# Optimization experiments

Hardware: AMD Instinct MI355X
Metric: run time of the kernel (lower is better)

The kernel has to match this reference:

```python
import jax, jax.numpy as jnp
import numpy as np
from jax.scipy.special import logsumexp

B, N, C = 64, 1024, 558
NUM_ITERS = 20
TEMP = 1.0
CLASS_W = 1.0
ASSIGN_W = 0.5
NEG_INF = -1e30  # grad-safe stand-in for float('-inf') used by the torch code
EPS = 1e-8


def setup_inputs() -> dict:
    key = jax.random.key(0)
    k1, k2, k3, k4 = jax.random.split(key, 4)
    logits = jax.random.normal(k1, (B, N, C), dtype=jnp.float32)
    labels = jax.random.randint(k2, (B, N), 0, C, dtype=jnp.int32)
    visible_mask = jax.random.uniform(k3, (B, N)) < 0.9
    visible_mask = visible_mask.at[:, 0].set(True)  # every worm has >=1 visible node
    dustbin_score = jnp.asarray(-1.0, dtype=jnp.float32)  # nn.Parameter(-1.0)
    return {"logits": logits, "dustbin_score": dustbin_score,
            "labels": labels, "visible_mask": visible_mask}


def _log_sinkhorn(log_scores, log_mu, log_nu, iters):
    # log_scores: [B, N, M]; log_mu: [B, N]; log_nu: [B, M]
    log_u0 = jnp.zeros(log_scores.shape[:2], jnp.float32)
    log_v0 = jnp.zeros((log_scores.shape[0], log_scores.shape[2]), jnp.float32)

    def step(carry, _):
        log_u, log_v = carry
        log_u = log_mu - logsumexp(log_scores + log_v[:, None, :], axis=-1)
        log_v = log_nu - logsumexp(log_scores + log_u[:, :, None], axis=1)
        return (log_u, log_v), None

    (log_u, log_v), _ = jax.lax.scan(step, (log_u0, log_v0), None, length=iters)
    return jnp.exp(log_scores + log_u[:, :, None] + log_v[:, None, :])


def reference(logits, dustbin_score, labels, visible_mask):
    log_probs = jax.nn.log_softmax(logits, axis=-1)  # [B, N, C]

    # ---- Matcher (one_to_one=False) ----
    log_scores = log_probs / TEMP
    dust = jnp.broadcast_to(dustbin_score / TEMP, (B, N, 1))
    ls = jnp.concatenate([log_scores, dust], axis=-1)  # [B, N, C+1]

    maskf = visible_mask.astype(jnp.float32)
    nvis = maskf.sum(axis=1)  # [B], >= 1 by construction
    log_mu = jnp.where(visible_mask, -jnp.log(nvis)[:, None], NEG_INF)  # [B, N]
    log_nu = jnp.full((B, C + 1), -jnp.log(jnp.float32(C + 1)))  # uniform marginals

    P = _log_sinkhorn(ls, log_mu, log_nu, NUM_ITERS)  # [B, N, C+1]
    soft = P[:, :, :-1]  # drop dustbin column -> [B, N, C]

    # ---- classification loss (worm-averaged NLL, label_smoothing=0) ----
    # labels are packed at the front: visible node with rank r uses labels[b, r]
    ranks = jnp.clip(jnp.cumsum(visible_mask.astype(jnp.int32), axis=1) - 1, 0)
    tgt = jnp.take_along_axis(labels, ranks, axis=1)  # [B, N]
    nll = -jnp.take_along_axis(log_probs, tgt[..., None], axis=2)[..., 0]  # [B, N]
    class_loss = ((nll * maskf).sum(axis=1) / nvis).mean()

    # ---- assignment confidence loss (worm-averaged entropy) ----
    ent = -(soft * jnp.log(soft + EPS)).sum(axis=-1)  # [B, N]
    assignment_loss = ((ent * maskf).sum(axis=1) / nvis).mean()

    total_loss = CLASS_W * class_loss + ASSIGN_W * assignment_loss
    return total_loss


if __name__ == "__main__":
    print(reference(**setup_inputs()))
```

## Files before the change

### kernel.cpp

```cpp
#include <hip/hip_runtime.h>

#define Bb 64
#define Nn 1024
#define Cc 558
#define CP1 559
#define CPAD 560
#define ITERS 20
#define PBLK 8
#define RPB (Nn/PBLK)
#define WAVES 8
#define RPW (RPB/WAVES)
#define BLOCK 512

#if __has_builtin(__builtin_amdgcn_rcpf)
#define RCP(x) __builtin_amdgcn_rcpf(x)
#else
#define RCP(x) (1.0f / (x))
#endif

__device__ __forceinline__ float wave_sum(float v) {
#pragma unroll
    for (int off = 32; off > 0; off >>= 1) v += __shfl_xor(v, off, 64);
    return v;
}
__device__ __forceinline__ float wave_max(float v) {
#pragma unroll
    for (int off = 32; off > 0; off >>= 1) v = fmaxf(v, __shfl_xor(v, off, 64));
    return v;
}

#if __has_builtin(__builtin_amdgcn_cvt_pk_fp8_f32) && __has_builtin(__builtin_amdgcn_cvt_pk_f32_fp8)
#define HW_FP8 1
typedef float v2f __attribute__((ext_vector_type(2)));
#endif

__device__ __forceinline__ unsigned enc1_sw(float v) {
    if (!(v > 0.f)) return 0u;
    unsigned u = __float_as_uint(v);
    unsigned t = u + 0x7FFFFu + ((u >> 20) & 1u);
    int e = (int)(t >> 23) - 120;
    if (e < 1) return 0u;
    if (e > 15) return 0x7Eu;
    return ((unsigned)e << 3) | ((t >> 20) & 7u);
}
__device__ __forceinline__ float dec1_sw(unsigned b8) {
    return b8 ? __uint_as_float((((b8 >> 3) + 120u) << 23) | ((b8 & 7u) << 20)) : 0.f;
}
__device__ __forceinline__ unsigned enc4(float f0, float f1, float f2, float f3) {
#ifdef HW_FP8
    int w = 0;
    w = __builtin_amdgcn_cvt_pk_fp8_f32(f0, f1, w, false);
    w = __builtin_amdgcn_cvt_pk_fp8_f32(f2, f3, w, true);
    return (unsigned)w;
#else
    return enc1_sw(f0) | (enc1_sw(f1) << 8) | (enc1_sw(f2) << 16) | (enc1_sw(f3) << 24);
#endif
}
__device__ __forceinline__ void dec4(unsigned w, float& f0, float& f1, float& f2, float& f3) {
#ifdef HW_FP8
    v2f a = __builtin_amdgcn_cvt_pk_f32_fp8((int)w, false);
    v2f b = __builtin_amdgcn_cvt_pk_f32_fp8((int)w, true);
    f0 = a[0]; f1 = a[1]; f2 = b[0]; f3 = b[1];
#else
    f0 = dec1_sw(w & 0xffu); f1 = dec1_sw((w >> 8) & 0xffu);
    f2 = dec1_sw((w >> 16) & 0xffu); f3 = dec1_sw(w >> 24);
#endif
}
__device__ __forceinline__ float dec1(unsigned b8) {
#ifdef HW_FP8
    v2f a = __builtin_amdgcn_cvt_pk_f32_fp8((int)b8, false);
    return a[0];
#else
    return dec1_sw(b8);
#endif
}

__global__ __launch_bounds__(256) void k0_softmax(const float* __restrict__ logits,
        const float* __restrict__ dustbin, unsigned char* __restrict__ p8,
        float* __restrict__ qd, float* __restrict__ lse) {
    const int wave = threadIdx.x >> 6, lane = threadIdx.x & 63;
    const int r = (blockIdx.x << 2) + wave;
    const float* rowp = logits + (size_t)r * Cc;
    const bool tl = lane < 46;
    const float e0 = __expf(rowp[lane]);
    const float e1 = __expf(rowp[64 + lane]);
    const float e2 = __expf(rowp[128 + lane]);
    const float e3 = __expf(rowp[192 + lane]);
    const float e4 = __expf(rowp[256 + lane]);
    const float e5 = __expf(rowp[320 + lane]);
    const float e6 = __expf(rowp[384 + lane]);
    const float e7 = __expf(rowp[448 + lane]);
    float et = 0.f;
    if (tl) et = __expf(rowp[512 + lane]);
    float mx = fmaxf(fmaxf(fmaxf(e0, e1), fmaxf(e2, e3)),
                     fmaxf(fmaxf(e4, e5), fmaxf(e6, e7)));
    mx = wave_max(fmaxf(mx, et));
    const float s = wave_sum(e0 + e1 + e2 + e3 + e4 + e5 + e6 + e7 + et);
    const float fm = 416.f * RCP(mx);
    const unsigned w0 = enc4(e0 * fm, e1 * fm, e2 * fm, e3 * fm);
    const unsigned w1 = enc4(e4 * fm, e5 * fm, e6 * fm, e7 * fm);
    unsigned char* rowq = p8 + (size_t)r * CPAD;
    *(unsigned long long*)(rowq + (lane << 3)) =
        (unsigned long long)w0 | ((unsigned long long)w1 << 32);
    if (tl) rowq[512 + lane] = (unsigned char)(enc4(et * fm, 0.f, 0.f, 0.f) & 0xffu);
    if (lane == 0) {
        qd[r] = __expf(dustbin[0]) * fm * s;
        lse[r] = __logf(s);
    }
}

__global__ __launch_bounds__(256) void k1_batch(const float* __restrict__ logits,
        const int* __restrict__ labels, const void* __restrict__ maskp,
        const float* __restrict__ lse, float* __restrict__ class_part,
        float* __restrict__ inv_nvis, unsigned char* __restrict__ visc) {
    const int b = blockIdx.x, tid = threadIdx.x;
    __shared__ int sF, sB;
    __shared__ int cs_[256];
    __shared__ float red[256];
    if (tid == 0) { sF = 0; sB = 0; }
    __syncthreads();
    {
        const unsigned int* mw = (const unsigned int*)maskp;
        int lF = 0, lB = 0;
        for (int i = tid; i < (Bb * Nn) / 4; i += 256) {
            unsigned w = mw[i];
            if (w == 0x3F800000u) lF = 1;
            else if (w > 1u) lB = 1;
        }
        if (lF) sF = 1;
        if (lB) sB = 1;
    }
    __syncthreads();
    const int mode = sF ? 2 : (sB ? 1 : 0);
    int v[4]; int local = 0;
#pragma unroll
    for (int j = 0; j < 4; ++j) {
        const int n = tid * 4 + j;
        const int idx = b * Nn + n;
        int m;
        if (mode == 1)      m = ((const unsigned char*)maskp)[idx] != 0;
        else if (mode == 2) m = ((const float*)maskp)[idx] != 0.f;
        else                m = ((const int*)maskp)[idx] != 0;
        v[j] = m; local += m;
    }
    cs_[tid] = local;
    __syncthreads();
    for (int off = 1; off < 256; off <<= 1) {
        int x = 0;
        if (tid >= off) x = cs_[tid - off];
        __syncthreads();
        cs_[tid] += x;
        __syncthreads();
    }
    const int nvis = cs_[255];
    int run = cs_[tid] - local;
    float nllsum = 0.f;
#pragma unroll
    for (int j = 0; j < 4; ++j) {
        const int n = tid * 4 + j;
        run += v[j];
        visc[b * Nn + n] = (unsigned char)v[j];
        if (v[j]) {
            const int tgt = labels[b * Nn + (run - 1)];
            nllsum += lse[b * Nn + n] - logits[((size_t)(b * Nn + n)) * Cc + tgt];
        }
    }
    red[tid] = nllsum;
    __syncthreads();
    for (int off = 128; off > 0; off >>= 1) {
        if (tid < off) red[tid] += red[tid + off];
        __syncthreads();
    }
    if (tid == 0) {
        class_part[b] = red[0] / (float)nvis;
        inv_nvis[b] = 1.f / (float)nvis;
    }
}

__global__ __launch_bounds__(BLOCK) void k2_iter(const unsigned char* __restrict__ p8,
        const float* __restrict__ qd, const unsigned char* __restrict__ visc,
        const float* __restrict__ inv_nvis, float* __restrict__ eu_g,
        const float* __restrict__ Rp, float* __restrict__ Wp, const int first) {
    __shared__ float evl[CPAD];
    __shared__ float partl[WAVES][CPAD];
    const int b = blockIdx.x >> 3, p = blockIdx.x & 7, tid = threadIdx.x;
    const int wave = tid >> 6, lane = tid & 63;
    for (int c = tid; c < CP1; c += BLOCK) {
        float ev = 1.f;
        if (!first) {
            const float* CSr = Rp + (size_t)(b * PBLK) * CPAD + c;
            float s = 0.f;
#pragma unroll
            for (int q = 0; q < PBLK; ++q) s += CSr[q * CPAD];
            ev = RCP(559.f * s);
        }
        evl[c] = ev;
    }
    __syncthreads();
    const bool tl = lane < 46;
    const float evr0 = evl[lane],        evr1 = evl[64 + lane];
    const float evr2 = evl[128 + lane],  evr3 = evl[192 + lane];
    const float evr4 = evl[256 + lane],  evr5 = evl[320 + lane];
    const float evr6 = evl[384 + lane],  evr7 = evl[448 + lane];
    const float evt = tl ? evl[512 + lane] : 0.f;
    const float evd = evl[558];
    const float invn = inv_nvis[b];
    const int row0 = (b << 10) + (p << 7) + (wave << 4);
    const uint4 vA = *(const uint4*)(visc + row0);
    const unsigned vw[4] = {vA.x, vA.y, vA.z, vA.w};
#define VISB(r) ((vw[(r) >> 2] >> (((r) & 3) << 3)) & 0xffu)
    float pc0 = 0.f, pc1 = 0.f, pc2 = 0.f, pc3 = 0.f;
    float pc4 = 0.f, pc5 = 0.f, pc6 = 0.f, pc7 = 0.f;
    float pct = 0.f, pcd = 0.f;
#pragma unroll
    for (int r = 0; r < RPW; ++r) {
        const unsigned char* rowq = p8 + (size_t)(row0 + r) * CPAD;
        const unsigned long long wq = *(const unsigned long long*)(rowq + (lane << 3));
        float f0, f1, f2, f3, f4, f5, f6, f7;
        dec4((unsigned)wq, f0, f1, f2, f3);
        dec4((unsigned)(wq >> 32), f4, f5, f6, f7);
        float xt = 0.f;
        if (tl) xt = dec1(rowq[512 + lane]);
        const float qdr = qd[row0 + r];
        float s = f0 * evr0 + f1 * evr1 + f2 * evr2 + f3 * evr3
                + f4 * evr4 + f5 * evr5 + f6 * evr6 + f7 * evr7 + xt * evt;
        s = wave_sum(s) + qdr * evd;
        const float euv = VISB(r) ? invn * RCP(s) : 0.f;
        if (lane == 0) eu_g[row0 + r] = euv;
        pc0 += f0 * euv; pc1 += f1 * euv; pc2 += f2 * euv; pc3 += f3 * euv;
        pc4 += f4 * euv; pc5 += f5 * euv; pc6 += f6 * euv; pc7 += f7 * euv;
        pct += xt * euv; pcd += qdr * euv;
    }
    partl[wave][lane] = pc0;        partl[wave][64 + lane] = pc1;
    partl[wave][128 + lane] = pc2;  partl[wave][192 + lane] = pc3;
    partl[wave][256 + lane] = pc4;  partl[wave][320 + lane] = pc5;
    partl[wave][384 + lane] = pc6;  partl[wave][448 + lane] = pc7;
    if (tl) partl[wave][512 + lane] = pct;
    if (lane == 0) partl[wave][558] = pcd;
    __syncthreads();
    float* CSw = Wp + (size_t)(b * PBLK + p) * CPAD;
    for (int c = tid; c < CP1; c += BLOCK) {
        CSw[c] = partl[0][c] + partl[1][c] + partl[2][c] + partl[3][c]
               + partl[4][c] + partl[5][c] + partl[6][c] + partl[7][c];
    }
}

__global__ __launch_bounds__(BLOCK) void k3_final(const unsigned char* __restrict__ p8,
        const float* __restrict__ eu_g, const float* __restrict__ Rp,
        const float* __restrict__ inv_nvis, float* __restrict__ assign_part) {
    __shared__ float evl[CPAD];
    __shared__ float red[WAVES];
    const int b = blockIdx.x >> 3, p = blockIdx.x & 7, tid = threadIdx.x;
    const int wave = tid >> 6, lane = tid & 63;
    for (int c = tid; c < CP1; c += BLOCK) {
        const float* CSr = Rp + (size_t)(b * PBLK) * CPAD + c;
        float s = 0.f;
#pragma unroll
        for (int q = 0; q < PBLK; ++q) s += CSr[q * CPAD];
        evl[c] = RCP(559.f * s);
    }
    __syncthreads();
    const bool tl = lane < 46;
    const float evr0 = evl[lane],        evr1 = evl[64 + lane];
    const float evr2 = evl[128 + lane],  evr3 = evl[192 + lane];
    const float evr4 = evl[256 + lane],  evr5 = evl[320 + lane];
    const float evr6 = evl[384 + lane],  evr7 = evl[448 + lane];
    const float evt = tl ? evl[512 + lane] : 0.f;
    const int row0 = (b << 10) + (p << 7) + (wave << 4);
    float acc = 0.f;
#pragma unroll
    for (int r = 0; r < RPW; ++r) {
        const float euv = eu_g[row0 + r];
        const unsigned char* rowq = p8 + (size_t)(row0 + r) * CPAD;
        const unsigned long long wq = *(const unsigned long long*)(rowq + (lane << 3));
        float f0, f1, f2, f3, f4, f5, f6, f7;
        dec4((unsigned)wq, f0, f1, f2, f3);
        dec4((unsigned)(wq >> 32), f4, f5, f6, f7);
        float xt = 0.f;
        if (tl) xt = dec1(rowq[512 + lane]);
        float P;
        P = f0 * euv * evr0; acc -= P * __logf(P + 1e-8f);
        P = f1 * euv * evr1; acc -= P * __logf(P + 1e-8f);
        P = f2 * euv * evr2; acc -= P * __logf(P + 1e-8f);
        P = f3 * euv * evr3; acc -= P * __logf(P + 1e-8f);
        P = f4 * euv * evr4; acc -= P * __logf(P + 1e-8f);
        P = f5 * euv * evr5; acc -= P * __logf(P + 1e-8f);
        P = f6 * euv * evr6; acc -= P * __logf(P + 1e-8f);
        P = f7 * euv * evr7; acc -= P * __logf(P + 1e-8f);
        P = xt * euv * evt;  acc -= P * __logf(P + 1e-8f);
    }
    acc = wave_sum(acc);
    if (lane == 0) red[wave] = acc;
    __syncthreads();
    if (tid == 0) {
        float s = 0.f;
#pragma unroll
        for (int w = 0; w < WAVES; ++w) s += red[w];
        assign_part[blockIdx.x] = s * inv_nvis[b];
    }
}

__global__ void k4_out(const float* __restrict__ class_part,
                       const float* __restrict__ assign_part, float* __restrict__ out) {
    const int b = threadIdx.x;
    float v = class_part[b];
    float a = 0.f;
#pragma unroll
    for (int p = 0; p < PBLK; ++p) a += assign_part[b * PBLK + p];
    v += 0.5f * a;
    v = wave_sum(v);
    if (b == 0) out[0] = v * (1.f / 64.f);
}

extern "C" void kernel_launch(void* const* d_in, const int* in_sizes, int n_in,
                              void* d_out, int out_size, void* d_ws, size_t ws_size,
                              hipStream_t stream) {
    const float* logits = (const float*)d_in[0];
    const float* dustbin = (const float*)d_in[1];
    const int* labels = (const int*)d_in[2];
    const void* mask = d_in[3];
    float* out = (float*)d_out;

    char* ws = (char*)d_ws;
    size_t off = 0;
    unsigned char* p8 = (unsigned char*)(ws + off); off += (size_t)Bb * Nn * CPAD;
    float* qd = (float*)(ws + off);            off += (size_t)Bb * Nn * 4;
    float* lse = (float*)(ws + off);           off += (size_t)Bb * Nn * 4;
    float* eu_g = (float*)(ws + off);          off += (size_t)Bb * Nn * 4;
    unsigned char* visc = (unsigned char*)(ws + off); off += (size_t)Bb * Nn;
    float* inv_nvis = (float*)(ws + off);      off += Bb * 4;
    float* parts = (float*)(ws + off);         off += 2ull * Bb * PBLK * CPAD * 4;
    float* class_part = (float*)(ws + off);    off += Bb * 4;
    float* assign_part = (float*)(ws + off);   off += Bb * PBLK * 4;
    const size_t SLOT = (size_t)Bb * PBLK * CPAD;

    k0_softmax<<<(Bb * Nn) / 4, 256, 0, stream>>>(logits, dustbin, p8, qd, lse);
    k1_batch<<<Bb, 256, 0, stream>>>(logits, labels, mask, lse,
                                     class_part, inv_nvis, visc);
    for (int t = 0; t < ITERS; ++t) {
        float* Wb = parts + (size_t)(t & 1) * SLOT;
        const float* Rb = parts + (size_t)((t + 1) & 1) * SLOT;
        k2_iter<<<Bb * PBLK, BLOCK, 0, stream>>>(p8, qd, visc, inv_nvis, eu_g, Rb, Wb,
                                                 (t == 0) ? 1 : 0);
    }
    k3_final<<<Bb * PBLK, BLOCK, 0, stream>>>(p8, eu_g,
            parts + (size_t)((ITERS - 1) & 1) * SLOT, inv_nvis, assign_part);
    k4_out<<<1, 64, 0, stream>>>(class_part, assign_part, out);
    (void)in_sizes; (void)n_in; (void)out_size; (void)ws_size;
}
```

Measured before the change: 572.7 us.

## Fuse softmax, class loss, Sinkhorn iterations and entropy into one per-batch kernel

Replaces the softmax, batch-stats, 20 per-iteration and final kernels with one persistent kernel: one 1024-thread block per batch. Column partial sums, row scalings, lse and dustbin terms now live in LDS instead of global memory. This removes about 20 kernel launches and the global round-trips of the partial sums, and skips invisible rows in the Sinkhorn and entropy loops. In exchange only 64 blocks run, so most of the GPU's compute units sit idle and each block must stream its whole batch of encoded scores on every iteration.

```diff
diff --git a/kernel.cpp b/kernel.cpp
--- a/kernel.cpp
+++ b/kernel.cpp
@@ -6,11 +6,8 @@
 #define CP1 559
 #define CPAD 560
 #define ITERS 20
-#define PBLK 8
-#define RPB (Nn/PBLK)
-#define WAVES 8
-#define RPW (RPB/WAVES)
-#define BLOCK 512
+#define NW 16
+#define BLOCK 1024
 
 #if __has_builtin(__builtin_amdgcn_rcpf)
 #define RCP(x) __builtin_amdgcn_rcpf(x)
@@ -75,55 +72,34 @@
 #endif
 }
 
-__global__ __launch_bounds__(256) void k0_softmax(const float* __restrict__ logits,
-        const float* __restrict__ dustbin, unsigned char* __restrict__ p8,
-        float* __restrict__ qd, float* __restrict__ lse) {
-    const int wave = threadIdx.x >> 6, lane = threadIdx.x & 63;
-    const int r = (blockIdx.x << 2) + wave;
-    const float* rowp = logits + (size_t)r * Cc;
+__global__ __launch_bounds__(BLOCK) void k_fused(
+        const float* __restrict__ logits, const float* __restrict__ dustbin,
+        const int* __restrict__ labels, const void* __restrict__ maskp,
+        unsigned char* __restrict__ p8, float* __restrict__ contrib) {
+    __shared__ float partl[NW][CPAD];
+    __shared__ float evl[CPAD];
+    __shared__ float lse_l[Nn];
+    __shared__ float eu_l[Nn];
+    __shared__ float qd_l[Nn];
+    __shared__ unsigned char visc_l[Nn];
+    __shared__ int cs_[Nn];
+    __shared__ float redL[NW];
+    __shared__ int sF, sB;
+    __shared__ float sClass, sInvn;
+
+    const int b = blockIdx.x, tid = threadIdx.x;
+    const int wave = tid >> 6, lane = tid & 63;
     const bool tl = lane < 46;
-    const float e0 = __expf(rowp[lane]);
-    const float e1 = __expf(rowp[64 + lane]);
-    const float e2 = __expf(rowp[128 + lane]);
-    const float e3 = __expf(rowp[192 + lane]);
-    const float e4 = __expf(rowp[256 + lane]);
-    const float e5 = __expf(rowp[320 + lane]);
-    const float e6 = __expf(rowp[384 + lane]);
-    const float e7 = __expf(rowp[448 + lane]);
-    float et = 0.f;
-    if (tl) et = __expf(rowp[512 + lane]);
-    float mx = fmaxf(fmaxf(fmaxf(e0, e1), fmaxf(e2, e3)),
-                     fmaxf(fmaxf(e4, e5), fmaxf(e6, e7)));
-    mx = wave_max(fmaxf(mx, et));
-    const float s = wave_sum(e0 + e1 + e2 + e3 + e4 + e5 + e6 + e7 + et);
-    const float fm = 416.f * RCP(mx);
-    const unsigned w0 = enc4(e0 * fm, e1 * fm, e2 * fm, e3 * fm);
-    const unsigned w1 = enc4(e4 * fm, e5 * fm, e6 * fm, e7 * fm);
-    unsigned char* rowq = p8 + (size_t)r * CPAD;
-    *(unsigned long long*)(rowq + (lane << 3)) =
-        (unsigned long long)w0 | ((unsigned long long)w1 << 32);
-    if (tl) rowq[512 + lane] = (unsigned char)(enc4(et * fm, 0.f, 0.f, 0.f) & 0xffu);
-    if (lane == 0) {
-        qd[r] = __expf(dustbin[0]) * fm * s;
-        lse[r] = __logf(s);
-    }
-}
-
-__global__ __launch_bounds__(256) void k1_batch(const float* __restrict__ logits,
-        const int* __restrict__ labels, const void* __restrict__ maskp,
-        const float* __restrict__ lse, float* __restrict__ class_part,
-        float* __restrict__ inv_nvis, unsigned char* __restrict__ visc) {
-    const int b = blockIdx.x, tid = threadIdx.x;
-    __shared__ int sF, sB;
-    __shared__ int cs_[256];
-    __shared__ float red[256];
+    const float dustp = __expf(dustbin[0]);
+
     if (tid == 0) { sF = 0; sB = 0; }
     __syncthreads();
     {
         const unsigned int* mw = (const unsigned int*)maskp;
         int lF = 0, lB = 0;
-        for (int i = tid; i < (Bb * Nn) / 4; i += 256) {
-            unsigned w = mw[i];
+#pragma unroll
+        for (int k = 0; k < 4; ++k) {
+            unsigned w = mw[tid + (k << 10)];
             if (w == 0x3F800000u) lF = 1;
             else if (w > 1u) lB = 1;
         }
@@ -132,184 +108,185 @@
     }
     __syncthreads();
     const int mode = sF ? 2 : (sB ? 1 : 0);
-    int v[4]; int local = 0;
-#pragma unroll
-    for (int j = 0; j < 4; ++j) {
-        const int n = tid * 4 + j;
-        const int idx = b * Nn + n;
-        int m;
-        if (mode == 1)      m = ((const unsigned char*)maskp)[idx] != 0;
-        else if (mode == 2) m = ((const float*)maskp)[idx] != 0.f;
-        else                m = ((const int*)maskp)[idx] != 0;
-        v[j] = m; local += m;
-    }
-    cs_[tid] = local;
-    __syncthreads();
-    for (int off = 1; off < 256; off <<= 1) {
-        int x = 0;
-        if (tid >= off) x = cs_[tid - off];
+
+    int vis_me;
+    {
+        const int idx = (b << 10) + tid;
+        if (mode == 1)      vis_me = ((const unsigned char*)maskp)[idx] != 0;
+        else if (mode == 2) vis_me = ((const float*)maskp)[idx] != 0.f;
+        else                vis_me = ((const int*)maskp)[idx] != 0;
+    }
+    visc_l[tid] = (unsigned char)vis_me;
+    cs_[tid] = vis_me;
+    __syncthreads();
+    for (int off = 1; off < BLOCK; off <<= 1) {
+        int x = (tid >= off) ? cs_[tid - off] : 0;
         __syncthreads();
         cs_[tid] += x;
         __syncthreads();
     }
-    const int nvis = cs_[255];
-    int run = cs_[tid] - local;
-    float nllsum = 0.f;
-#pragma unroll
-    for (int j = 0; j < 4; ++j) {
-        const int n = tid * 4 + j;
-        run += v[j];
-        visc[b * Nn + n] = (unsigned char)v[j];
-        if (v[j]) {
-            const int tgt = labels[b * Nn + (run - 1)];
-            nllsum += lse[b * Nn + n] - logits[((size_t)(b * Nn + n)) * Cc + tgt];
-        }
-    }
-    red[tid] = nllsum;
-    __syncthreads();
-    for (int off = 128; off > 0; off >>= 1) {
-        if (tid < off) red[tid] += red[tid + off];
-        __syncthreads();
-    }
+    if (tid == 0) sInvn = 1.f / (float)cs_[Nn - 1];
+
+#pragma unroll 1
+    for (int r = 0; r < 64; ++r) {
+        const int row = (wave << 6) + r;
+        const float* rowp = logits + ((size_t)(b << 10) + row) * Cc;
+        const float e0 = __expf(rowp[lane]);
+        const float e1 = __expf(rowp[64 + lane]);
+        const float e2 = __expf(rowp[128 + lane]);
+        const float e3 = __expf(rowp[192 + lane]);
+        const float e4 = __expf(rowp[256 + lane]);
+        const float e5 = __expf(rowp[320 + lane]);
+        const float e6 = __expf(rowp[384 + lane]);
+        const float e7 = __expf(rowp[448 + lane]);
+        float et = 0.f;
+        if (tl) et = __expf(rowp[512 + lane]);
+        float mx = fmaxf(fmaxf(fmaxf(e0, e1), fmaxf(e2, e3)),
+                         fmaxf(fmaxf(e4, e5), fmaxf(e6, e7)));
+        mx = wave_max(fmaxf(mx, et));
+        const float s = wave_sum(e0 + e1 + e2 + e3 + e4 + e5 + e6 + e7 + et);
+        const float fm = 416.f * RCP(mx);
+        const unsigned w0 = enc4(e0 * fm, e1 * fm, e2 * fm, e3 * fm);
+        const unsigned w1 = enc4(e4 * fm, e5 * fm, e6 * fm, e7 * fm);
+        unsigned char* rowq = p8 + ((size_t)(b << 10) + row) * CPAD;
+        *(unsigned long long*)(rowq + (lane << 3)) =
+            (unsigned long long)w0 | ((unsigned long long)w1 << 32);
+        if (tl) rowq[512 + lane] = (unsigned char)(enc4(et * fm, 0.f, 0.f, 0.f) & 0xffu);
+        if (lane == 0) {
+            lse_l[row] = __logf(s);
+            qd_l[row] = dustp * fm * s;
+        }
+    }
+    __syncthreads();
+
+    {
+        float nll = 0.f;
+        if (vis_me) {
+            const int tgt = labels[(b << 10) + (cs_[tid] - 1)];
+            nll = lse_l[tid] - logits[((size_t)(b << 10) + tid) * Cc + tgt];
+        }
+        nll = wave_sum(nll);
+        if (lane == 0) redL[wave] = nll;
+        __syncthreads();
+        if (tid == 0) {
+            float s = 0.f;
+#pragma unroll
+            for (int w = 0; w < NW; ++w) s += redL[w];
+            sClass = s;
+        }
+    }
+    const unsigned long long vmask = __ballot(visc_l[(wave << 6) + lane] != 0);
+    __syncthreads();
+    const float invn = sInvn;
+
+    for (int t = 0; t < ITERS; ++t) {
+        if (tid < CP1) {
+            float ev = 1.f;
+            if (t) {
+                float s = 0.f;
+#pragma unroll
+                for (int w = 0; w < NW; ++w) s += partl[w][tid];
+                ev = RCP(559.f * s);
+            }
+            evl[tid] = ev;
+        }
+        __syncthreads();
+        const float evr0 = evl[lane],        evr1 = evl[64 + lane];
+        const float evr2 = evl[128 + lane],  evr3 = evl[192 + lane];
+        const float evr4 = evl[256 + lane],  evr5 = evl[320 + lane];
+        const float evr6 = evl[384 + lane],  evr7 = evl[448 + lane];
+        const float evt = tl ? evl[512 + lane] : 0.f;
+        const float evd = evl[558];
+        float pc0 = 0.f, pc1 = 0.f, pc2 = 0.f, pc3 = 0.f;
+        float pc4 = 0.f, pc5 = 0.f, pc6 = 0.f, pc7 = 0.f;
+        float pct = 0.f, pcd = 0.f;
+#pragma unroll 2
+        for (int r = 0; r < 64; ++r) {
+            const int row = (wave << 6) + r;
+            if ((vmask >> r) & 1ull) {
+                const unsigned char* rowq = p8 + ((size_t)(b << 10) + row) * CPAD;
+                const unsigned long long wq =
+                    *(const unsigned long long*)(rowq + (lane << 3));
+                float f0, f1, f2, f3, f4, f5, f6, f7;
+                dec4((unsigned)wq, f0, f1, f2, f3);
+                dec4((unsigned)(wq >> 32), f4, f5, f6, f7);
+                float xt = 0.f;
+                if (tl) xt = dec1(rowq[512 + lane]);
+                const float qdr = qd_l[row];
+                float s = f0 * evr0 + f1 * evr1 + f2 * evr2 + f3 * evr3
+                        + f4 * evr4 + f5 * evr5 + f6 * evr6 + f7 * evr7 + xt * evt;
+                s = wave_sum(s) + qdr * evd;
+                const float euv = invn * RCP(s);
+                if (lane == 0) eu_l[row] = euv;
+                pc0 += f0 * euv; pc1 += f1 * euv; pc2 += f2 * euv; pc3 += f3 * euv;
+                pc4 += f4 * euv; pc5 += f5 * euv; pc6 += f6 * euv; pc7 += f7 * euv;
+                pct += xt * euv; pcd += qdr * euv;
+            } else if (lane == 0) {
+                eu_l[row] = 0.f;
+            }
+        }
+        partl[wave][lane] = pc0;        partl[wave][64 + lane] = pc1;
+        partl[wave][128 + lane] = pc2;  partl[wave][192 + lane] = pc3;
+        partl[wave][256 + lane] = pc4;  partl[wave][320 + lane] = pc5;
+        partl[wave][384 + lane] = pc6;  partl[wave][448 + lane] = pc7;
+        if (tl) partl[wave][512 + lane] = pct;
+        if (lane == 0) partl[wave][558] = pcd;
+        __syncthreads();
+    }
+
+    if (tid < CP1) {
+        float s = 0.f;
+#pragma unroll
+        for (int w = 0; w < NW; ++w) s += partl[w][tid];
+        evl[tid] = RCP(559.f * s);
+    }
+    __syncthreads();
+    {
+        const float evr0 = evl[lane],        evr1 = evl[64 + lane];
+        const float evr2 = evl[128 + lane],  evr3 = evl[192 + lane];
+        const float evr4 = evl[256 + lane],  evr5 = evl[320 + lane];
+        const float evr6 = evl[384 + lane],  evr7 = evl[448 + lane];
+        const float evt = tl ? evl[512 + lane] : 0.f;
+        float acc = 0.f;
+#pragma unroll 1
+        for (int r = 0; r < 64; ++r) {
+            if (!((vmask >> r) & 1ull)) continue;
+            const int row = (wave << 6) + r;
+            const float euv = eu_l[row];
+            const unsigned char* rowq = p8 + ((size_t)(b << 10) + row) * CPAD;
+            const unsigned long long wq = *(const unsigned long long*)(rowq + (lane << 3));
+            float f0, f1, f2, f3, f4, f5, f6, f7;
+            dec4((unsigned)wq, f0, f1, f2, f3);
+            dec4((unsigned)(wq >> 32), f4, f5, f6, f7);
+            float xt = 0.f;
+            if (tl) xt = dec1(rowq[512 + lane]);
+            float P;
+            P = f0 * euv * evr0; acc -= P * __logf(P + 1e-8f);
+            P = f1 * euv * evr1; acc -= P * __logf(P + 1e-8f);
+            P = f2 * euv * evr2; acc -= P * __logf(P + 1e-8f);
+            P = f3 * euv * evr3; acc -= P * __logf(P + 1e-8f);
+            P = f4 * euv * evr4; acc -= P * __logf(P + 1e-8f);
+            P = f5 * euv * evr5; acc -= P * __logf(P + 1e-8f);
+            P = f6 * euv * evr6; acc -= P * __logf(P + 1e-8f);
+            P = f7 * euv * evr7; acc -= P * __logf(P + 1e-8f);
+            P = xt * euv * evt;  acc -= P * __logf(P + 1e-8f);
+        }
+        acc = wave_sum(acc);
+        if (lane == 0) redL[wave] = acc;
+    }
+    __syncthreads();
     if (tid == 0) {
-        class_part[b] = red[0] / (float)nvis;
-        inv_nvis[b] = 1.f / (float)nvis;
-    }
-}
-
-__global__ __launch_bounds__(BLOCK) void k2_iter(const unsigned char* __restrict__ p8,
-        const float* __restrict__ qd, const unsigned char* __restrict__ visc,
-        const float* __restrict__ inv_nvis, float* __restrict__ eu_g,
-        const float* __restrict__ Rp, float* __restrict__ Wp, const int first) {
-    __shared__ float evl[CPAD];
-    __shared__ float partl[WAVES][CPAD];
-    const int b = blockIdx.x >> 3, p = blockIdx.x & 7, tid = threadIdx.x;
-    const int wave = tid >> 6, lane = tid & 63;
-    for (int c = tid; c < CP1; c += BLOCK) {
-        float ev = 1.f;
-        if (!first) {
-            const float* CSr = Rp + (size_t)(b * PBLK) * CPAD + c;
-            float s = 0.f;
-#pragma unroll
-            for (int q = 0; q < PBLK; ++q) s += CSr[q * CPAD];
-            ev = RCP(559.f * s);
-        }
-        evl[c] = ev;
-    }
-    __syncthreads();
-    const bool tl = lane < 46;
-    const float evr0 = evl[lane],        evr1 = evl[64 + lane];
-    const float evr2 = evl[128 + lane],  evr3 = evl[192 + lane];
-    const float evr4 = evl[256 + lane],  evr5 = evl[320 + lane];
-    const float evr6 = evl[384 + lane],  evr7 = evl[448 + lane];
-    const float evt = tl ? evl[512 + lane] : 0.f;
-    const float evd = evl[558];
-    const float invn = inv_nvis[b];
-    const int row0 = (b << 10) + (p << 7) + (wave << 4);
-    const uint4 vA = *(const uint4*)(visc + row0);
-    const unsigned vw[4] = {vA.x, vA.y, vA.z, vA.w};
-#define VISB(r) ((vw[(r) >> 2] >> (((r) & 3) << 3)) & 0xffu)
-    float pc0 = 0.f, pc1 = 0.f, pc2 = 0.f, pc3 = 0.f;
-    float pc4 = 0.f, pc5 = 0.f, pc6 = 0.f, pc7 = 0.f;
-    float pct = 0.f, pcd = 0.f;
-#pragma unroll
-    for (int r = 0; r < RPW; ++r) {
-        const unsigned char* rowq = p8 + (size_t)(row0 + r) * CPAD;
-        const unsigned long long wq = *(const unsigned long long*)(rowq + (lane << 3));
-        float f0, f1, f2, f3, f4, f5, f6, f7;
-        dec4((unsigned)wq, f0, f1, f2, f3);
-        dec4((unsigned)(wq >> 32), f4, f5, f6, f7);
-        float xt = 0.f;
-        if (tl) xt = dec1(rowq[512 + lane]);
-        const float qdr = qd[row0 + r];
-        float s = f0 * evr0 + f1 * evr1 + f2 * evr2 + f3 * evr3
-                + f4 * evr4 + f5 * evr5 + f6 * evr6 + f7 * evr7 + xt * evt;
-        s = wave_sum(s) + qdr * evd;
-        const float euv = VISB(r) ? invn * RCP(s) : 0.f;
-        if (lane == 0) eu_g[row0 + r] = euv;
-        pc0 += f0 * euv; pc1 += f1 * euv; pc2 += f2 * euv; pc3 += f3 * euv;
-        pc4 += f4 * euv; pc5 += f5 * euv; pc6 += f6 * euv; pc7 += f7 * euv;
-        pct += xt * euv; pcd += qdr * euv;
-    }
-    partl[wave][lane] = pc0;        partl[wave][64 + lane] = pc1;
-    partl[wave][128 + lane] = pc2;  partl[wave][192 + lane] = pc3;
-    partl[wave][256 + lane] = pc4;  partl[wave][320 + lane] = pc5;
-    partl[wave][384 + lane] = pc6;  partl[wave][448 + lane] = pc7;
-    if (tl) partl[wave][512 + lane] = pct;
-    if (lane == 0) partl[wave][558] = pcd;
-    __syncthreads();
-    float* CSw = Wp + (size_t)(b * PBLK + p) * CPAD;
-    for (int c = tid; c < CP1; c += BLOCK) {
-        CSw[c] = partl[0][c] + partl[1][c] + partl[2][c] + partl[3][c]
-               + partl[4][c] + partl[5][c] + partl[6][c] + partl[7][c];
-    }
-}
-
-__global__ __launch_bounds__(BLOCK) void k3_final(const unsigned char* __restrict__ p8,
-        const float* __restrict__ eu_g, const float* __restrict__ Rp,
-        const float* __restrict__ inv_nvis, float* __restrict__ assign_part) {
-    __shared__ float evl[CPAD];
-    __shared__ float red[WAVES];
-    const int b = blockIdx.x >> 3, p = blockIdx.x & 7, tid = threadIdx.x;
-    const int wave = tid >> 6, lane = tid & 63;
-    for (int c = tid; c < CP1; c += BLOCK) {
-        const float* CSr = Rp + (size_t)(b * PBLK) * CPAD + c;
-        float s = 0.f;
-#pragma unroll
-        for (int q = 0; q < PBLK; ++q) s += CSr[q * CPAD];
-        evl[c] = RCP(559.f * s);
-    }
-    __syncthreads();
-    const bool tl = lane < 46;
-    const float evr0 = evl[lane],        evr1 = evl[64 + lane];
-    const float evr2 = evl[128 + lane],  evr3 = evl[192 + lane];
-    const float evr4 = evl[256 + lane],  evr5 = evl[320 + lane];
-    const float evr6 = evl[384 + lane],  evr7 = evl[448 + lane];
-    const float evt = tl ? evl[512 + lane] : 0.f;
-    const int row0 = (b << 10) + (p << 7) + (wave << 4);
-    float acc = 0.f;
-#pragma unroll
-    for (int r = 0; r < RPW; ++r) {
-        const float euv = eu_g[row0 + r];
-        const unsigned char* rowq = p8 + (size_t)(row0 + r) * CPAD;
-        const unsigned long long wq = *(const unsigned long long*)(rowq + (lane << 3));
-        float f0, f1, f2, f3, f4, f5, f6, f7;
-        dec4((unsigned)wq, f0, f1, f2, f3);
-        dec4((unsigned)(wq >> 32), f4, f5, f6, f7);
-        float xt = 0.f;
-        if (tl) xt = dec1(rowq[512 + lane]);
-        float P;
-        P = f0 * euv * evr0; acc -= P * __logf(P + 1e-8f);
-        P = f1 * euv * evr1; acc -= P * __logf(P + 1e-8f);
-        P = f2 * euv * evr2; acc -= P * __logf(P + 1e-8f);
-        P = f3 * euv * evr3; acc -= P * __logf(P + 1e-8f);
-        P = f4 * euv * evr4; acc -= P * __logf(P + 1e-8f);
-        P = f5 * euv * evr5; acc -= P * __logf(P + 1e-8f);
-        P = f6 * euv * evr6; acc -= P * __logf(P + 1e-8f);
-        P = f7 * euv * evr7; acc -= P * __logf(P + 1e-8f);
-        P = xt * euv * evt;  acc -= P * __logf(P + 1e-8f);
-    }
-    acc = wave_sum(acc);
-    if (lane == 0) red[wave] = acc;
-    __syncthreads();
-    if (tid == 0) {
-        float s = 0.f;
-#pragma unroll
-        for (int w = 0; w < WAVES; ++w) s += red[w];
-        assign_part[blockIdx.x] = s * inv_nvis[b];
-    }
-}
-
-__global__ void k4_out(const float* __restrict__ class_part,
-                       const float* __restrict__ assign_part, float* __restrict__ out) {
-    const int b = threadIdx.x;
-    float v = class_part[b];
-    float a = 0.f;
-#pragma unroll
-    for (int p = 0; p < PBLK; ++p) a += assign_part[b * PBLK + p];
-    v += 0.5f * a;
+        float ent = 0.f;
+#pragma unroll
+        for (int w = 0; w < NW; ++w) ent += redL[w];
+        contrib[b] = (sClass + 0.5f * ent) * sInvn;
+    }
+}
+
+__global__ void k4_out(const float* __restrict__ contrib, float* __restrict__ out) {
+    float v = contrib[threadIdx.x];
     v = wave_sum(v);
-    if (b == 0) out[0] = v * (1.f / 64.f);
+    if (threadIdx.x == 0) out[0] = v * (1.f / 64.f);
 }
 
 extern "C" void kernel_launch(void* const* d_in, const int* in_sizes, int n_in,
@@ -324,27 +301,9 @@
     char* ws = (char*)d_ws;
     size_t off = 0;
     unsigned char* p8 = (unsigned char*)(ws + off); off += (size_t)Bb * Nn * CPAD;
-    float* qd = (float*)(ws + off);            off += (size_t)Bb * Nn * 4;
-    float* lse = (float*)(ws + off);           off += (size_t)Bb * Nn * 4;
-    float* eu_g = (float*)(ws + off);          off += (size_t)Bb * Nn * 4;
-    unsigned char* visc = (unsigned char*)(ws + off); off += (size_t)Bb * Nn;
-    float* inv_nvis = (float*)(ws + off);      off += Bb * 4;
-    float* parts = (float*)(ws + off);         off += 2ull * Bb * PBLK * CPAD * 4;
-    float* class_part = (float*)(ws + off);    off += Bb * 4;
-    float* assign_part = (float*)(ws + off);   off += Bb * PBLK * 4;
-    const size_t SLOT = (size_t)Bb * PBLK * CPAD;
-
-    k0_softmax<<<(Bb * Nn) / 4, 256, 0, stream>>>(logits, dustbin, p8, qd, lse);
-    k1_batch<<<Bb, 256, 0, stream>>>(logits, labels, mask, lse,
-                                     class_part, inv_nvis, visc);
-    for (int t = 0; t < ITERS; ++t) {
-        float* Wb = parts + (size_t)(t & 1) * SLOT;
-        const float* Rb = parts + (size_t)((t + 1) & 1) * SLOT;
-        k2_iter<<<Bb * PBLK, BLOCK, 0, stream>>>(p8, qd, visc, inv_nvis, eu_g, Rb, Wb,
-                                                 (t == 0) ? 1 : 0);
-    }
-    k3_final<<<Bb * PBLK, BLOCK, 0, stream>>>(p8, eu_g,
-            parts + (size_t)((ITERS - 1) & 1) * SLOT, inv_nvis, assign_part);
-    k4_out<<<1, 64, 0, stream>>>(class_part, assign_part, out);
+    float* contrib = (float*)(ws + off);            off += Bb * 4;
+
+    k_fused<<<Bb, BLOCK, 0, stream>>>(logits, dustbin, labels, mask, p8, contrib);
+    k4_out<<<1, 64, 0, stream>>>(contrib, out);
     (void)in_sizes; (void)n_in; (void)out_size; (void)ws_size;
 }
```

Measured after the change: 892.3 us. 55.8% more time.

## Fuse all Sinkhorn iterations and entropy into one persistent per-batch kernel

Applied to the files above, without the earlier changes.

Replaces the 20 per-iteration launches and the separate final-entropy kernel with one kernel that runs one 1024-thread block per batch. Column partial sums, row scalings, marginals and visibility stay in LDS across iterations, so the global partial-sum buffers, the eu_g buffer and the inter-kernel round trips go away. Row loads are batched eight at a time for memory-level parallelism, and the wave reductions switch to DPP with a readlane. The cost is that only 64 blocks run, each on one CU, so each CU has to stream its batch's FP8 matrix 21 times with far less parallelism than the earlier 512-block grid.

```diff
diff --git a/kernel.cpp b/kernel.cpp
--- a/kernel.cpp
+++ b/kernel.cpp
@@ -6,11 +6,8 @@
 #define CP1 559
 #define CPAD 560
 #define ITERS 20
-#define PBLK 8
-#define RPB (Nn/PBLK)
-#define WAVES 8
-#define RPW (RPB/WAVES)
-#define BLOCK 512
+#define NW 16
+#define BLOCK 1024
 
 #if __has_builtin(__builtin_amdgcn_rcpf)
 #define RCP(x) __builtin_amdgcn_rcpf(x)
@@ -18,6 +15,31 @@
 #define RCP(x) (1.0f / (x))
 #endif
 
+#if __has_builtin(__builtin_amdgcn_update_dpp) && __has_builtin(__builtin_amdgcn_readlane)
+template <int CTRL>
+__device__ __forceinline__ float dpp_mv(float x) {
+    return __int_as_float(
+        __builtin_amdgcn_update_dpp(0, __float_as_int(x), CTRL, 0xf, 0xf, true));
+}
+__device__ __forceinline__ float wave_sum(float x) {
+    x += dpp_mv<0x111>(x);
+    x += dpp_mv<0x112>(x);
+    x += dpp_mv<0x114>(x);
+    x += dpp_mv<0x118>(x);
+    x += dpp_mv<0x142>(x);
+    x += dpp_mv<0x143>(x);
+    return __int_as_float(__builtin_amdgcn_readlane(__float_as_int(x), 63));
+}
+__device__ __forceinline__ float wave_max(float x) {
+    x = fmaxf(x, dpp_mv<0x111>(x));
+    x = fmaxf(x, dpp_mv<0x112>(x));
+    x = fmaxf(x, dpp_mv<0x114>(x));
+    x = fmaxf(x, dpp_mv<0x118>(x));
+    x = fmaxf(x, dpp_mv<0x142>(x));
+    x = fmaxf(x, dpp_mv<0x143>(x));
+    return __int_as_float(__builtin_amdgcn_readlane(__float_as_int(x), 63));
+}
+#else
 __device__ __forceinline__ float wave_sum(float v) {
 #pragma unroll
     for (int off = 32; off > 0; off >>= 1) v += __shfl_xor(v, off, 64);
@@ -28,6 +50,7 @@
     for (int off = 32; off > 0; off >>= 1) v = fmaxf(v, __shfl_xor(v, off, 64));
     return v;
 }
+#endif
 
 #if __has_builtin(__builtin_amdgcn_cvt_pk_fp8_f32) && __has_builtin(__builtin_amdgcn_cvt_pk_f32_fp8)
 #define HW_FP8 1
@@ -68,10 +91,10 @@
 }
 __device__ __forceinline__ float dec1(unsigned b8) {
 #ifdef HW_FP8
-    v2f a = __builtin_amdgcn_cvt_pk_f32_fp8((int)b8, false);
+    v2f a = __builtin_amdgcn_cvt_pk_f32_fp8((int)(b8 & 0xffu), false);
     return a[0];
 #else
-    return dec1_sw(b8);
+    return dec1_sw(b8 & 0xffu);
 #endif
 }
 
@@ -177,137 +200,142 @@
     }
 }
 
-__global__ __launch_bounds__(BLOCK) void k2_iter(const unsigned char* __restrict__ p8,
-        const float* __restrict__ qd, const unsigned char* __restrict__ visc,
-        const float* __restrict__ inv_nvis, float* __restrict__ eu_g,
-        const float* __restrict__ Rp, float* __restrict__ Wp, const int first) {
+__global__ __launch_bounds__(BLOCK) void k_iter(
+        const unsigned char* __restrict__ p8, const float* __restrict__ qd,
+        const unsigned char* __restrict__ visc, const float* __restrict__ inv_nvis,
+        float* __restrict__ assign_part) {
+    __shared__ float partl[NW][CPAD];
     __shared__ float evl[CPAD];
-    __shared__ float partl[WAVES][CPAD];
-    const int b = blockIdx.x >> 3, p = blockIdx.x & 7, tid = threadIdx.x;
+    __shared__ float qd_l[Nn];
+    __shared__ float vf_l[Nn];
+    __shared__ float eu_l[Nn];
+    __shared__ float redE[NW];
+    const int b = blockIdx.x, tid = threadIdx.x;
     const int wave = tid >> 6, lane = tid & 63;
-    for (int c = tid; c < CP1; c += BLOCK) {
-        float ev = 1.f;
-        if (!first) {
-            const float* CSr = Rp + (size_t)(b * PBLK) * CPAD + c;
-            float s = 0.f;
-#pragma unroll
-            for (int q = 0; q < PBLK; ++q) s += CSr[q * CPAD];
-            ev = RCP(559.f * s);
-        }
-        evl[c] = ev;
-    }
-    __syncthreads();
     const bool tl = lane < 46;
-    const float evr0 = evl[lane],        evr1 = evl[64 + lane];
-    const float evr2 = evl[128 + lane],  evr3 = evl[192 + lane];
-    const float evr4 = evl[256 + lane],  evr5 = evl[320 + lane];
-    const float evr6 = evl[384 + lane],  evr7 = evl[448 + lane];
-    const float evt = tl ? evl[512 + lane] : 0.f;
-    const float evd = evl[558];
     const float invn = inv_nvis[b];
-    const int row0 = (b << 10) + (p << 7) + (wave << 4);
-    const uint4 vA = *(const uint4*)(visc + row0);
-    const unsigned vw[4] = {vA.x, vA.y, vA.z, vA.w};
-#define VISB(r) ((vw[(r) >> 2] >> (((r) & 3) << 3)) & 0xffu)
-    float pc0 = 0.f, pc1 = 0.f, pc2 = 0.f, pc3 = 0.f;
-    float pc4 = 0.f, pc5 = 0.f, pc6 = 0.f, pc7 = 0.f;
-    float pct = 0.f, pcd = 0.f;
-#pragma unroll
-    for (int r = 0; r < RPW; ++r) {
-        const unsigned char* rowq = p8 + (size_t)(row0 + r) * CPAD;
-        const unsigned long long wq = *(const unsigned long long*)(rowq + (lane << 3));
-        float f0, f1, f2, f3, f4, f5, f6, f7;
-        dec4((unsigned)wq, f0, f1, f2, f3);
-        dec4((unsigned)(wq >> 32), f4, f5, f6, f7);
-        float xt = 0.f;
-        if (tl) xt = dec1(rowq[512 + lane]);
-        const float qdr = qd[row0 + r];
-        float s = f0 * evr0 + f1 * evr1 + f2 * evr2 + f3 * evr3
-                + f4 * evr4 + f5 * evr5 + f6 * evr6 + f7 * evr7 + xt * evt;
-        s = wave_sum(s) + qdr * evd;
-        const float euv = VISB(r) ? invn * RCP(s) : 0.f;
-        if (lane == 0) eu_g[row0 + r] = euv;
-        pc0 += f0 * euv; pc1 += f1 * euv; pc2 += f2 * euv; pc3 += f3 * euv;
-        pc4 += f4 * euv; pc5 += f5 * euv; pc6 += f6 * euv; pc7 += f7 * euv;
-        pct += xt * euv; pcd += qdr * euv;
-    }
-    partl[wave][lane] = pc0;        partl[wave][64 + lane] = pc1;
-    partl[wave][128 + lane] = pc2;  partl[wave][192 + lane] = pc3;
-    partl[wave][256 + lane] = pc4;  partl[wave][320 + lane] = pc5;
-    partl[wave][384 + lane] = pc6;  partl[wave][448 + lane] = pc7;
-    if (tl) partl[wave][512 + lane] = pct;
-    if (lane == 0) partl[wave][558] = pcd;
-    __syncthreads();
-    float* CSw = Wp + (size_t)(b * PBLK + p) * CPAD;
-    for (int c = tid; c < CP1; c += BLOCK) {
-        CSw[c] = partl[0][c] + partl[1][c] + partl[2][c] + partl[3][c]
-               + partl[4][c] + partl[5][c] + partl[6][c] + partl[7][c];
-    }
-}
-
-__global__ __launch_bounds__(BLOCK) void k3_final(const unsigned char* __restrict__ p8,
-        const float* __restrict__ eu_g, const float* __restrict__ Rp,
-        const float* __restrict__ inv_nvis, float* __restrict__ assign_part) {
-    __shared__ float evl[CPAD];
-    __shared__ float red[WAVES];
-    const int b = blockIdx.x >> 3, p = blockIdx.x & 7, tid = threadIdx.x;
-    const int wave = tid >> 6, lane = tid & 63;
-    for (int c = tid; c < CP1; c += BLOCK) {
-        const float* CSr = Rp + (size_t)(b * PBLK) * CPAD + c;
+    const unsigned char* qb = p8 + ((size_t)b << 10) * CPAD;
+
+    qd_l[tid] = qd[(b << 10) + tid];
+    vf_l[tid] = visc[(b << 10) + tid] ? invn : 0.f;
+    __syncthreads();
+
+    for (int t = 0; t < ITERS; ++t) {
+        if (tid < CP1) {
+            float ev = 1.f;
+            if (t) {
+                float s = 0.f;
+#pragma unroll
+                for (int w = 0; w < NW; ++w) s += partl[w][tid];
+                ev = RCP(559.f * s);
+            }
+            evl[tid] = ev;
+        }
+        __syncthreads();
+        const float evr0 = evl[lane],        evr1 = evl[64 + lane];
+        const float evr2 = evl[128 + lane],  evr3 = evl[192 + lane];
+        const float evr4 = evl[256 + lane],  evr5 = evl[320 + lane];
+        const float evr6 = evl[384 + lane],  evr7 = evl[448 + lane];
+        const float evt = tl ? evl[512 + lane] : 0.f;
+        const float evd = evl[558];
+        float pc0 = 0.f, pc1 = 0.f, pc2 = 0.f, pc3 = 0.f;
+        float pc4 = 0.f, pc5 = 0.f, pc6 = 0.f, pc7 = 0.f;
+        float pct = 0.f, pcd = 0.f;
+        for (int g = 0; g < 64; g += 8) {
+            unsigned long long wq[8];
+            unsigned tb[8];
+#pragma unroll
+            for (int j = 0; j < 8; ++j) {
+                const unsigned char* rowq = qb + (size_t)((wave << 6) + g + j) * CPAD;
+                wq[j] = *(const unsigned long long*)(rowq + (lane << 3));
+                tb[j] = rowq[512 + lane];
+            }
+#pragma unroll
+            for (int j = 0; j < 8; ++j) {
+                const int row = (wave << 6) + g + j;
+                float f0, f1, f2, f3, f4, f5, f6, f7;
+                dec4((unsigned)wq[j], f0, f1, f2, f3);
+                dec4((unsigned)(wq[j] >> 32), f4, f5, f6, f7);
+                const float xt = dec1(tb[j]);
+                float s = f0 * evr0 + f1 * evr1 + f2 * evr2 + f3 * evr3
+                        + f4 * evr4 + f5 * evr5 + f6 * evr6 + f7 * evr7 + xt * evt;
+                s = wave_sum(s);
+                const float qdr = qd_l[row];
+                const float euv = vf_l[row] * RCP(s + qdr * evd);
+                if (lane == 0) eu_l[row] = euv;
+                pc0 += f0 * euv; pc1 += f1 * euv; pc2 += f2 * euv; pc3 += f3 * euv;
+                pc4 += f4 * euv; pc5 += f5 * euv; pc6 += f6 * euv; pc7 += f7 * euv;
+                pct += xt * euv; pcd += qdr * euv;
+            }
+        }
+        partl[wave][lane] = pc0;        partl[wave][64 + lane] = pc1;
+        partl[wave][128 + lane] = pc2;  partl[wave][192 + lane] = pc3;
+        partl[wave][256 + lane] = pc4;  partl[wave][320 + lane] = pc5;
+        partl[wave][384 + lane] = pc6;  partl[wave][448 + lane] = pc7;
+        if (tl) partl[wave][512 + lane] = pct;
+        if (lane == 0) partl[wave][558] = pcd;
+        __syncthreads();
+    }
+
+    if (tid < CP1) {
         float s = 0.f;
 #pragma unroll
-        for (int q = 0; q < PBLK; ++q) s += CSr[q * CPAD];
-        evl[c] = RCP(559.f * s);
-    }
-    __syncthreads();
-    const bool tl = lane < 46;
-    const float evr0 = evl[lane],        evr1 = evl[64 + lane];
-    const float evr2 = evl[128 + lane],  evr3 = evl[192 + lane];
-    const float evr4 = evl[256 + lane],  evr5 = evl[320 + lane];
-    const float evr6 = evl[384 + lane],  evr7 = evl[448 + lane];
-    const float evt = tl ? evl[512 + lane] : 0.f;
-    const int row0 = (b << 10) + (p << 7) + (wave << 4);
-    float acc = 0.f;
-#pragma unroll
-    for (int r = 0; r < RPW; ++r) {
-        const float euv = eu_g[row0 + r];
-        const unsigned char* rowq = p8 + (size_t)(row0 + r) * CPAD;
-        const unsigned long long wq = *(const unsigned long long*)(rowq + (lane << 3));
-        float f0, f1, f2, f3, f4, f5, f6, f7;
-        dec4((unsigned)wq, f0, f1, f2, f3);
-        dec4((unsigned)(wq >> 32), f4, f5, f6, f7);
-        float xt = 0.f;
-        if (tl) xt = dec1(rowq[512 + lane]);
-        float P;
-        P = f0 * euv * evr0; acc -= P * __logf(P + 1e-8f);
-        P = f1 * euv * evr1; acc -= P * __logf(P + 1e-8f);
-        P = f2 * euv * evr2; acc -= P * __logf(P + 1e-8f);
-        P = f3 * euv * evr3; acc -= P * __logf(P + 1e-8f);
-        P = f4 * euv * evr4; acc -= P * __logf(P + 1e-8f);
-        P = f5 * euv * evr5; acc -= P * __logf(P + 1e-8f);
-        P = f6 * euv * evr6; acc -= P * __logf(P + 1e-8f);
-        P = f7 * euv * evr7; acc -= P * __logf(P + 1e-8f);
-        P = xt * euv * evt;  acc -= P * __logf(P + 1e-8f);
-    }
-    acc = wave_sum(acc);
-    if (lane == 0) red[wave] = acc;
+        for (int w = 0; w < NW; ++w) s += partl[w][tid];
+        evl[tid] = RCP(559.f * s);
+    }
+    __syncthreads();
+    {
+        const float evr0 = evl[lane],        evr1 = evl[64 + lane];
+        const float evr2 = evl[128 + lane],  evr3 = evl[192 + lane];
+        const float evr4 = evl[256 + lane],  evr5 = evl[320 + lane];
+        const float evr6 = evl[384 + lane],  evr7 = evl[448 + lane];
+        const float evt = tl ? evl[512 + lane] : 0.f;
+        float acc = 0.f;
+        for (int g = 0; g < 64; g += 4) {
+            unsigned long long wq[4];
+            unsigned tb[4];
+#pragma unroll
+            for (int j = 0; j < 4; ++j) {
+                const unsigned char* rowq = qb + (size_t)((wave << 6) + g + j) * CPAD;
+                wq[j] = *(const unsigned long long*)(rowq + (lane << 3));
+                tb[j] = rowq[512 + lane];
+            }
+#pragma unroll
+            for (int j = 0; j < 4; ++j) {
+                const int row = (wave << 6) + g + j;
+                const float euv = eu_l[row];
+                float f0, f1, f2, f3, f4, f5, f6, f7;
+                dec4((unsigned)wq[j], f0, f1, f2, f3);
+                dec4((unsigned)(wq[j] >> 32), f4, f5, f6, f7);
+                const float xt = dec1(tb[j]);
+                float P;
+                P = f0 * euv * evr0; acc -= P * __logf(P + 1e-8f);
+                P = f1 * euv * evr1; acc -= P * __logf(P + 1e-8f);
+                P = f2 * euv * evr2; acc -= P * __logf(P + 1e-8f);
+                P = f3 * euv * evr3; acc -= P * __logf(P + 1e-8f);
+                P = f4 * euv * evr4; acc -= P * __logf(P + 1e-8f);
+                P = f5 * euv * evr5; acc -= P * __logf(P + 1e-8f);
+                P = f6 * euv * evr6; acc -= P * __logf(P + 1e-8f);
+                P = f7 * euv * evr7; acc -= P * __logf(P + 1e-8f);
+                P = xt * euv * evt;  acc -= P * __logf(P + 1e-8f);
+            }
+        }
+        acc = wave_sum(acc);
+        if (lane == 0) redE[wave] = acc;
+    }
     __syncthreads();
     if (tid == 0) {
-        float s = 0.f;
-#pragma unroll
-        for (int w = 0; w < WAVES; ++w) s += red[w];
-        assign_part[blockIdx.x] = s * inv_nvis[b];
+        float ent = 0.f;
+#pragma unroll
+        for (int w = 0; w < NW; ++w) ent += redE[w];
+        assign_part[b] = ent * invn;
     }
 }
 
 __global__ void k4_out(const float* __restrict__ class_part,
                        const float* __restrict__ assign_part, float* __restrict__ out) {
     const int b = threadIdx.x;
-    float v = class_part[b];
-    float a = 0.f;
-#pragma unroll
-    for (int p = 0; p < PBLK; ++p) a += assign_part[b * PBLK + p];
-    v += 0.5f * a;
+    float v = class_part[b] + 0.5f * assign_part[b];
     v = wave_sum(v);
     if (b == 0) out[0] = v * (1.f / 64.f);
 }
@@ -326,25 +354,15 @@
     unsigned char* p8 = (unsigned char*)(ws + off); off += (size_t)Bb * Nn * CPAD;
     float* qd = (float*)(ws + off);            off += (size_t)Bb * Nn * 4;
     float* lse = (float*)(ws + off);           off += (size_t)Bb * Nn * 4;
-    float* eu_g = (float*)(ws + off);          off += (size_t)Bb * Nn * 4;
     unsigned char* visc = (unsigned char*)(ws + off); off += (size_t)Bb * Nn;
     float* inv_nvis = (float*)(ws + off);      off += Bb * 4;
-    float* parts = (float*)(ws + off);         off += 2ull * Bb * PBLK * CPAD * 4;
     float* class_part = (float*)(ws + off);    off += Bb * 4;
-    float* assign_part = (float*)(ws + off);   off += Bb * PBLK * 4;
-    const size_t SLOT = (size_t)Bb * PBLK * CPAD;
+    float* assign_part = (float*)(ws + off);   off += Bb * 4;
 
     k0_softmax<<<(Bb * Nn) / 4, 256, 0, stream>>>(logits, dustbin, p8, qd, lse);
     k1_batch<<<Bb, 256, 0, stream>>>(logits, labels, mask, lse,
                                      class_part, inv_nvis, visc);
-    for (int t = 0; t < ITERS; ++t) {
-        float* Wb = parts + (size_t)(t & 1) * SLOT;
-        const float* Rb = parts + (size_t)((t + 1) & 1) * SLOT;
-        k2_iter<<<Bb * PBLK, BLOCK, 0, stream>>>(p8, qd, visc, inv_nvis, eu_g, Rb, Wb,
-                                                 (t == 0) ? 1 : 0);
-    }
-    k3_final<<<Bb * PBLK, BLOCK, 0, stream>>>(p8, eu_g,
-            parts + (size_t)((ITERS - 1) & 1) * SLOT, inv_nvis, assign_part);
+    k_iter<<<Bb, BLOCK, 0, stream>>>(p8, qd, visc, inv_nvis, assign_part);
     k4_out<<<1, 64, 0, stream>>>(class_part, assign_part, out);
     (void)in_sizes; (void)n_in; (void)out_size; (void)ws_size;
 }
```

Measured after the change: 618.8 us. 8.0% more time.
